# Optimization experiments

Hardware: AMD Instinct MI355X
Metric: run time of the kernel (lower is better)

The kernel has to match this reference:

```python
import jax, jax.numpy as jnp
import numpy as np

NUM_HEAD = 8   # in_channels // 64 for in_channels=512
DIM = 8        # per-head dim (== num_head in this module)
H_CH = NUM_HEAD * DIM  # 64
SCALE = DIM ** (-0.5)


def _conv(x, w, b, padding):
    # x: [N,C,H,W], w: [O,I,kh,kw]
    out = jax.lax.conv_general_dilated(
        x, w, window_strides=(1, 1), padding=padding,
        dimension_numbers=("NCHW", "OIHW", "NCHW"))
    return out + b[None, :, None, None]


def setup_inputs() -> dict:
    key = jax.random.key(0)
    ks = jax.random.split(key, 4)
    N, C, H, W = 4, 512, 48, 48
    x = jax.random.normal(ks[0], (N, C, H, W), dtype=jnp.float32)
    qkv_w = jax.random.normal(ks[1], (3 * H_CH, C, 1, 1), dtype=jnp.float32) * 0.05
    qkv_b = jnp.zeros((3 * H_CH,), dtype=jnp.float32)
    pos_w = jax.random.normal(ks[2], (H_CH, H_CH, 3, 3), dtype=jnp.float32) * 0.05
    pos_b = jnp.zeros((H_CH,), dtype=jnp.float32)
    res_w = jax.random.normal(ks[3], (C, H_CH, 1, 1), dtype=jnp.float32) * 0.05
    res_b = jnp.zeros((C,), dtype=jnp.float32)
    return {"x": x, "qkv_w": qkv_w, "qkv_b": qkv_b,
            "pos_w": pos_w, "pos_b": pos_b,
            "res_w": res_w, "res_b": res_b}


def reference(x, qkv_w, qkv_b, pos_w, pos_b, res_w, res_b):
    N, C, H, W = x.shape
    L = H * W
    # 1x1 conv QKV projection -> [N, 3h, H, W]
    qkv = _conv(x, qkv_w, qkv_b, "VALID")
    # [N, num_head, 3*dim, L]
    qkv = qkv.reshape(N, NUM_HEAD, 3 * DIM, L)
    q, k, v = qkv[:, :, :DIM], qkv[:, :, DIM:2 * DIM], qkv[:, :, 2 * DIM:]
    # attn = q^T @ k * scale : [N, nh, L, L], softmax over keys (last dim)
    attn = jnp.einsum("nhdq,nhdk->nhqk", q, k) * SCALE
    attn = jax.nn.softmax(attn, axis=-1)
    # out = v @ attn^T : [N, nh, dim, L]
    out = jnp.einsum("nhdk,nhqk->nhdq", v, attn)
    out = out.reshape(N, H_CH, H, W)
    # positional branch: 3x3 conv on v
    pos = _conv(v.reshape(N, H_CH, H, W), pos_w, pos_b, "SAME")
    out = out + pos
    # resume 1x1 conv -> [N, out_channels, H, W]
    return _conv(out, res_w, res_b, "VALID")
```

## Files before the change

### kernel.cpp

```cpp
#include <hip/hip_runtime.h>

#define L_ATT 2304
#define QSCALE_LOG2E 0.5100695712f

using bh8 = __attribute__((ext_vector_type(8))) short;
using f4  = __attribute__((ext_vector_type(4))) float;

#if __has_builtin(__builtin_amdgcn_exp2f)
#define EXP2(x) __builtin_amdgcn_exp2f(x)
#else
#define EXP2(x) exp2f(x)
#endif

__device__ inline short f2b(float f) {
    union { float f; unsigned u; } c; c.f = f;
    unsigned r = (c.u + 0x7FFFu + ((c.u >> 16) & 1u)) >> 16;
    return (short)r;
}
__device__ inline float b2f(short s) {
    union { unsigned u; float f; } c;
    c.u = ((unsigned)(unsigned short)s) << 16;
    return c.f;
}
__device__ inline int packhi(float lo, float hi) {
    return (int)__builtin_amdgcn_perm(__float_as_uint(hi), __float_as_uint(lo), 0x07060302u);
}
__device__ inline unsigned pk2(float lo, float hi) {
    return (unsigned)(unsigned short)f2b(lo) | ((unsigned)(unsigned short)f2b(hi) << 16);
}

__global__ __launch_bounds__(256) void prep_kernel(
    const float* __restrict__ qkv_w, const float* __restrict__ res_w,
    const float* __restrict__ pos_w, short* __restrict__ wqb,
    short* __restrict__ reswb, short* __restrict__ wqp)
{
    int j = blockIdx.x * 256 + threadIdx.x;
    if (j < 24576) {
        float4 v = ((const float4*)qkv_w)[j];
        short4 o = { f2b(v.x), f2b(v.y), f2b(v.z), f2b(v.w) };
        *(short4*)(wqb + (size_t)j * 4) = o;
    } else if (j < 32768) {
        int idx = j - 24576;
        float4 v = ((const float4*)res_w)[idx];
        short4 o = { f2b(v.x), f2b(v.y), f2b(v.z), f2b(v.w) };
        *(short4*)(reswb + (size_t)idx * 4) = o;
    } else {
        int e = j - 32768;
        wqp[e] = f2b(pos_w[(size_t)(e & 4095) * 9 + (e >> 12)]);
    }
}

__global__ __launch_bounds__(256) void qkv_kernel(
    const float* __restrict__ x, const short* __restrict__ wqb,
    const float* __restrict__ qkv_b, short* __restrict__ qt8,
    short* __restrict__ kt8, short* __restrict__ vt, short* __restrict__ vle)
{
    __shared__ short bs[32 * 520];
    const int g = blockIdx.x;
    const int xcd = g & 7, rr = g >> 3;
    const int y = rr % 3, grp = rr / 3;
    const int code = grp * 8 + xcd;
    const int l0 = (code % 72) * 32, oc0 = y * 64, n = code / 72;

    const int tid = threadIdx.x;
    const int lane = tid & 63, wave = tid >> 6;
    const int col = lane & 15, quad = lane >> 4;
    const int ocb = oc0 + wave * 16;

    {
        const float* src = x + (size_t)n * 512 * L_ATT + l0;
#pragma unroll
        for (int j = 0; j < 8; ++j) {
            int idx = j * 256 + tid;
            int k2 = (idx >> 3) * 2;
            int lq = (idx & 7) * 4;
            float4 av = *(const float4*)(src + (size_t)k2 * L_ATT + lq);
            float4 bv = *(const float4*)(src + (size_t)(k2 + 1) * L_ATT + lq);
            *(unsigned*)&bs[(lq + 0) * 520 + k2] = pk2(av.x, bv.x);
            *(unsigned*)&bs[(lq + 1) * 520 + k2] = pk2(av.y, bv.y);
            *(unsigned*)&bs[(lq + 2) * 520 + k2] = pk2(av.z, bv.z);
            *(unsigned*)&bs[(lq + 3) * 520 + k2] = pk2(av.w, bv.w);
        }
    }
    __syncthreads();

    f4 acc[2];
    acc[0] = (f4){0.f, 0.f, 0.f, 0.f};
    acc[1] = (f4){0.f, 0.f, 0.f, 0.f};

    const short* arow = wqb + (size_t)(ocb + col) * 512 + quad * 8;
    const short* b0p = bs + col * 520 + quad * 8;
    const short* b1p = b0p + 16 * 520;

#pragma unroll 4
    for (int k0 = 0; k0 < 512; k0 += 32) {
        bh8 af = *(const bh8*)(arow + k0);
        bh8 b0 = *(const bh8*)(b0p + k0);
        bh8 b1 = *(const bh8*)(b1p + k0);
        acc[0] = __builtin_amdgcn_mfma_f32_16x16x32_bf16(af, b0, acc[0], 0, 0, 0);
        acc[1] = __builtin_amdgcn_mfma_f32_16x16x32_bf16(af, b1, acc[1], 0, 0, 0);
    }

    const int obase = ocb + quad * 4;
    const int h = obase / 24;
    const int r0 = obase - h * 24;
    const int slice = n * 8 + h;

#pragma unroll
    for (int nt = 0; nt < 2; ++nt) {
        int l = l0 + nt * 16 + col;
        float v[4];
#pragma unroll
        for (int reg = 0; reg < 4; ++reg) v[reg] = acc[nt][reg] + qkv_b[obase + reg];
        if (r0 < 8) {
            short4 o = { f2b(v[0] * QSCALE_LOG2E), f2b(v[1] * QSCALE_LOG2E),
                         f2b(v[2] * QSCALE_LOG2E), f2b(v[3] * QSCALE_LOG2E) };
            *(short4*)(qt8 + ((size_t)slice * L_ATT + l) * 8 + r0) = o;
        } else if (r0 < 16) {
            short4 o = { f2b(v[0]), f2b(v[1]), f2b(v[2]), f2b(v[3]) };
            *(short4*)(kt8 + ((size_t)slice * L_ATT + l) * 8 + (r0 - 8)) = o;
        } else {
            short4 o = { f2b(v[0]), f2b(v[1]), f2b(v[2]), f2b(v[3]) };
            int d0 = r0 - 16;
#pragma unroll
            for (int reg = 0; reg < 4; ++reg)
                vt[((size_t)slice * 8 + d0 + reg) * L_ATT + l] = ((short*)&o)[reg];
            *(short4*)(vle + ((size_t)n * L_ATT + l) * 64 + h * 8 + d0) = o;
        }
    }
}

__global__ __launch_bounds__(256) void attnpos_kernel(
    const short* __restrict__ qt8, const short* __restrict__ kt8,
    const short* __restrict__ vt, const short* __restrict__ vle,
    const short* __restrict__ wqp, const float* __restrict__ pbias,
    float* __restrict__ pnum, float* __restrict__ pls, short* __restrict__ pcv)
{
    __shared__ short smem[6160];
    const int g = blockIdx.x;
    const int tid = threadIdx.x;
    const int lane = tid & 63, wave = tid >> 6;
    const int col = lane & 15, quad = lane >> 4;

    if (g < 1152) {
        const int h = g & 7, r = g >> 3;
        const int n = r / 36;
        const int rem = r - n * 36;
        const int qt = rem >> 1, half = rem & 1;
        const int q0 = qt * 128;
        const int kbase = half * 1152;
        const int slice = n * 8 + h;

        const short* qs  = qt8 + (size_t)slice * L_ATT * 8;
        const short* ks8 = kt8 + (size_t)slice * L_ATT * 8;
        const short* vb  = vt  + (size_t)slice * 8 * L_ATT;

        if (tid < 16) smem[6144 + tid] = (tid < 8) ? (short)0x3F80 : (short)0;

        bh8 zero8 = {0, 0, 0, 0, 0, 0, 0, 0};
        bh8 qf[2];
#pragma unroll
        for (int f = 0; f < 2; ++f) {
            qf[f] = zero8;
            if (quad == 0)
                qf[f] = *(const bh8*)(qs + (size_t)(q0 + wave * 32 + f * 16 + col) * 8);
        }

        int kidx[4];
#pragma unroll
        for (int nt = 0; nt < 4; ++nt)
            kidx[nt] = (quad == 0) ? (nt * 16 + col) * 8 : 6152;
        int vidx[2];
#pragma unroll
        for (int ks = 0; ks < 2; ++ks)
            vidx[ks] = (col < 8)
                     ? col * 64 + ((ks * 32 + quad * 8 + col * 8) & 63)
                     : ((col == 8) ? 6144 : 6152);

        const int ksl = ((lane >> 5) & 1) * 32 + ((lane >> 2) & 1) * 16
                      + ((lane >> 3) & 3) * 4 + (lane & 3);
        const int vd = lane >> 3, vkc = (lane & 7) * 8;
        const int vsl = vd * 64 + ((vkc + vd * 8) & 63);

        if (wave < 3)
            *(uint4*)&smem[wave * 512 + ksl * 8] =
                *(const uint4*)(ks8 + (size_t)(kbase + wave * 64 + lane) * 8);
        else
            *(uint4*)&smem[3072 + vsl] =
                *(const uint4*)(vb + (size_t)vd * L_ATT + kbase + vkc);
        if (wave == 0)
            *(uint4*)&smem[3072 + 512 + vsl] =
                *(const uint4*)(vb + (size_t)vd * L_ATT + kbase + 64 + vkc);
        else if (wave == 1)
            *(uint4*)&smem[3072 + 1024 + vsl] =
                *(const uint4*)(vb + (size_t)vd * L_ATT + kbase + 128 + vkc);
        __syncthreads();

        f4 oacc[2];
        oacc[0] = (f4){0.f, 0.f, 0.f, 0.f};
        oacc[1] = (f4){0.f, 0.f, 0.f, 0.f};

        int p = 0;
        for (int t = 0; t < 6; ++t) {
            uint4 dA, dB;
            if (wave < 3)
                dA = *(const uint4*)(ks8 + (size_t)(kbase + (t * 3 + 3 + wave) * 64 + lane) * 8);
            else
                dA = *(const uint4*)(vb + (size_t)vd * L_ATT + kbase + (t * 3 + 3) * 64 + vkc);
            if (wave == 0)
                dB = *(const uint4*)(vb + (size_t)vd * L_ATT + kbase + (t * 3 + 4) * 64 + vkc);
            else if (wave == 1)
                dB = *(const uint4*)(vb + (size_t)vd * L_ATT + kbase + (t * 3 + 5) * 64 + vkc);

#pragma unroll
            for (int u = 0; u < 3; ++u) {
                const int ku = (quad == 0) ? p * 1536 + u * 512 : 0;
                const int vu = (col < 8) ? 3072 + p * 1536 + u * 512 : 0;
                bh8 kf[4], vf[2];
#pragma unroll
                for (int nt = 0; nt < 4; ++nt) kf[nt] = *(const bh8*)&smem[kidx[nt] + ku];
#pragma unroll
                for (int ks = 0; ks < 2; ++ks) vf[ks] = *(const bh8*)&smem[vidx[ks] + vu];

                __builtin_amdgcn_s_setprio(1);
#pragma unroll
                for (int f = 0; f < 2; ++f) {
                    f4 s[4];
#pragma unroll
                    for (int nt = 0; nt < 4; ++nt) {
                        f4 z = (f4){0.f, 0.f, 0.f, 0.f};
                        s[nt] = __builtin_amdgcn_mfma_f32_16x16x32_bf16(kf[nt], qf[f], z, 0, 0, 0);
                    }
                    float e[4][4];
#pragma unroll
                    for (int nt = 0; nt < 4; ++nt)
#pragma unroll
                        for (int reg = 0; reg < 4; ++reg)
                            e[nt][reg] = EXP2(s[nt][reg]);
#pragma unroll
                    for (int ks = 0; ks < 2; ++ks) {
                        union { int i[4]; bh8 v; } pu;
                        pu.i[0] = packhi(e[2 * ks][0],     e[2 * ks][1]);
                        pu.i[1] = packhi(e[2 * ks][2],     e[2 * ks][3]);
                        pu.i[2] = packhi(e[2 * ks + 1][0], e[2 * ks + 1][1]);
                        pu.i[3] = packhi(e[2 * ks + 1][2], e[2 * ks + 1][3]);
                        oacc[f] = __builtin_amdgcn_mfma_f32_16x16x32_bf16(vf[ks], pu.v, oacc[f], 0, 0, 0);
                    }
                }
                __builtin_amdgcn_s_setprio(0);
            }

            if (wave < 3)
                *(uint4*)&smem[(p ^ 1) * 1536 + wave * 512 + ksl * 8] = dA;
            else
                *(uint4*)&smem[3072 + (p ^ 1) * 1536 + vsl] = dA;
            if (wave == 0)
                *(uint4*)&smem[3072 + (p ^ 1) * 1536 + 512 + vsl] = dB;
            else if (wave == 1)
                *(uint4*)&smem[3072 + (p ^ 1) * 1536 + 1024 + vsl] = dB;
            p ^= 1;
            __syncthreads();
        }

        const size_t prow = (size_t)(slice * 2 + half) * L_ATT;
#pragma unroll
        for (int f = 0; f < 2; ++f) {
            int qg = q0 + wave * 32 + f * 16 + col;
            if (quad < 2) {
                float4 o = { oacc[f][0], oacc[f][1], oacc[f][2], oacc[f][3] };
                *(float4*)(pnum + (prow + qg) * 8 + quad * 4) = o;
            } else if (quad == 2) {
                pls[prow + qg] = oacc[f][0];
            }
        }
        return;
    }

    const int gf = g - 1152;
    const int l0 = (gf % 144) * 16, n = gf / 144;
    const int t = wave;

    const int la = l0 + col;
    const int ya = la / 48, xa = la - ya * 48;

    f4 acc = (f4){0.f, 0.f, 0.f, 0.f};
    const short* vbase = vle + (size_t)n * L_ATT * 64;

#pragma unroll
    for (int q = 0; q < 9; ++q) {
        const int dy = q / 3 - 1, dx = q - (q / 3) * 3 - 1;
        const bool valid = ((unsigned)(ya + dy) < 48u) && ((unsigned)(xa + dx) < 48u);
        const short* ap = vbase + (size_t)(la + dy * 48 + dx) * 64 + quad * 8;
#pragma unroll
        for (int ks = 0; ks < 2; ++ks) {
            bh8 af = {0, 0, 0, 0, 0, 0, 0, 0};
            if (valid) af = *(const bh8*)(ap + ks * 32);
            bh8 bf = *(const bh8*)(wqp + ((size_t)q * 64 + t * 16 + col) * 64
                                   + ks * 32 + quad * 8);
            acc = __builtin_amdgcn_mfma_f32_16x16x32_bf16(af, bf, acc, 0, 0, 0);
        }
    }

    short* op = pcv + (size_t)n * L_ATT * 64;
    const int oc = t * 16 + col;
    const float bb = pbias[oc];
#pragma unroll
    for (int reg = 0; reg < 4; ++reg) {
        int l = l0 + quad * 4 + reg;
        op[(size_t)l * 64 + oc] = f2b(acc[reg] + bb);
    }
}

__global__ __launch_bounds__(256) void comb_kernel(
    const float* __restrict__ pnum, const float* __restrict__ pls,
    const short* __restrict__ pcv, short* __restrict__ battp)
{
    const int b = blockIdx.x;
    const int n = b / 144, lt = b % 144;
    const int hh = threadIdx.x & 15;
    const int l  = lt * 16 + (threadIdx.x >> 4);
    const int h = hh >> 1, dh = hh & 1;

    const size_t p0 = (size_t)((n * 8 + h) * 2) * L_ATT;
    const size_t p1 = p0 + L_ATT;
    float4 a = *(const float4*)(pnum + (p0 + l) * 8 + dh * 4);
    float4 c = *(const float4*)(pnum + (p1 + l) * 8 + dh * 4);
    float inv = 1.0f / (pls[p0 + l] + pls[p1 + l]);
    short4 pv = *(const short4*)(pcv + ((size_t)n * L_ATT + l) * 64 + hh * 4);

    int2 o;
    o.x = packhi((a.x + c.x) * inv + b2f(pv.x), (a.y + c.y) * inv + b2f(pv.y));
    o.y = packhi((a.z + c.z) * inv + b2f(pv.z), (a.w + c.w) * inv + b2f(pv.w));
    *(int2*)(battp + ((size_t)n * L_ATT + l) * 64 + hh * 4) = o;
}

__global__ __launch_bounds__(256) void res_kernel(
    const short* __restrict__ battp, const short* __restrict__ reswb,
    const float* __restrict__ res_b, float* __restrict__ out)
{
    const int g = blockIdx.x;
    const int xcd = g & 7, rr = g >> 3;
    const int y = rr & 7, grp = rr >> 3;
    const int code = grp * 8 + xcd;
    const int l0 = (code % 36) * 64, oc0 = y * 64, n = code / 36;

    const int lane = threadIdx.x & 63, wave = threadIdx.x >> 6;
    const int col = lane & 15, quad = lane >> 4;
    const int ocb = oc0 + wave * 16;

    f4 acc[4];
#pragma unroll
    for (int nt = 0; nt < 4; ++nt) acc[nt] = (f4){0.f, 0.f, 0.f, 0.f};

#pragma unroll
    for (int ks = 0; ks < 2; ++ks) {
        bh8 af = *(const bh8*)(reswb + (size_t)(ocb + col) * 64 + ks * 32 + quad * 8);
        const int ch = ks * 32 + quad * 8;
#pragma unroll
        for (int nt = 0; nt < 4; ++nt) {
            const int l = l0 + nt * 16 + col;
            bh8 bf = *(const bh8*)(battp + ((size_t)n * L_ATT + l) * 64 + ch);
            acc[nt] = __builtin_amdgcn_mfma_f32_16x16x32_bf16(af, bf, acc[nt], 0, 0, 0);
        }
    }

#pragma unroll
    for (int nt = 0; nt < 4; ++nt) {
        int l = l0 + nt * 16 + col;
#pragma unroll
        for (int reg = 0; reg < 4; ++reg) {
            int oc = ocb + quad * 4 + reg;
            out[((size_t)n * 512 + oc) * L_ATT + l] = acc[nt][reg] + res_b[oc];
        }
    }
}

extern "C" void kernel_launch(void* const* d_in, const int* in_sizes, int n_in,
                              void* d_out, int out_size, void* d_ws, size_t ws_size,
                              hipStream_t stream)
{
    const float* x      = (const float*)d_in[0];
    const float* qkv_w  = (const float*)d_in[1];
    const float* qkv_b  = (const float*)d_in[2];
    const float* pos_w  = (const float*)d_in[3];
    const float* pos_b  = (const float*)d_in[4];
    const float* res_w  = (const float*)d_in[5];
    const float* res_b  = (const float*)d_in[6];
    float* out = (float*)d_out;

    char* ws = (char*)d_ws;
    float* pnum  = (float*)(ws);
    float* pls   = (float*)(ws + 4718592);
    short* qt8   = (short*)(ws + 9437184);
    short* kt8   = (short*)(ws + 10616832);
    short* vt    = (short*)(ws + 11796480);
    short* pcv   = (short*)(ws + 12976128);
    short* wqb   = (short*)(ws + 14155776);
    short* reswb = (short*)(ws + 14352384);
    short* vle   = (short*)(ws + 14417920);
    short* wqp   = (short*)(ws + 15597568);
    short* battp = (short*)(ws + 15671296);

    prep_kernel<<<272, 256, 0, stream>>>(qkv_w, res_w, pos_w, wqb, reswb, wqp);
    qkv_kernel<<<864, 256, 0, stream>>>(x, wqb, qkv_b, qt8, kt8, vt, vle);
    attnpos_kernel<<<1728, 256, 0, stream>>>(qt8, kt8, vt, vle, wqp, pos_b, pnum, pls, pcv);
    comb_kernel<<<576, 256, 0, stream>>>(pnum, pls, pcv, battp);
    res_kernel<<<1152, 256, 0, stream>>>(battp, reswb, res_b, out);
}
```

Measured before the change: 132.4 us.

## Load whole K/V half-range into LDS once instead of double-buffered streaming

```diff
diff --git a/kernel.cpp b/kernel.cpp
--- a/kernel.cpp
+++ b/kernel.cpp
@@ -136,7 +136,7 @@
     const short* __restrict__ wqp, const float* __restrict__ pbias,
     float* __restrict__ pnum, float* __restrict__ pls, short* __restrict__ pcv)
 {
-    __shared__ short smem[6160];
+    __shared__ short smem[18448];
     const int g = blockIdx.x;
     const int tid = threadIdx.x;
     const int lane = tid & 63, wave = tid >> 6;
@@ -155,7 +155,7 @@
         const short* ks8 = kt8 + (size_t)slice * L_ATT * 8;
         const short* vb  = vt  + (size_t)slice * 8 * L_ATT;
 
-        if (tid < 16) smem[6144 + tid] = (tid < 8) ? (short)0x3F80 : (short)0;
+        if (tid < 16) smem[18432 + tid] = (tid < 8) ? (short)0x3F80 : (short)0;
 
         bh8 zero8 = {0, 0, 0, 0, 0, 0, 0, 0};
         bh8 qf[2];
@@ -169,97 +169,66 @@
         int kidx[4];
 #pragma unroll
         for (int nt = 0; nt < 4; ++nt)
-            kidx[nt] = (quad == 0) ? (nt * 16 + col) * 8 : 6152;
+            kidx[nt] = (quad == 0) ? (nt * 16 + col) * 8 : 18440;
         int vidx[2];
 #pragma unroll
         for (int ks = 0; ks < 2; ++ks)
             vidx[ks] = (col < 8)
-                     ? col * 64 + ((ks * 32 + quad * 8 + col * 8) & 63)
-                     : ((col == 8) ? 6144 : 6152);
+                     ? 9216 + col * 64 + ((ks * 32 + quad * 8 + col * 8) & 63)
+                     : ((col == 8) ? 18432 : 18440);
 
         const int ksl = ((lane >> 5) & 1) * 32 + ((lane >> 2) & 1) * 16
                       + ((lane >> 3) & 3) * 4 + (lane & 3);
         const int vd = lane >> 3, vkc = (lane & 7) * 8;
         const int vsl = vd * 64 + ((vkc + vd * 8) & 63);
 
-        if (wave < 3)
-            *(uint4*)&smem[wave * 512 + ksl * 8] =
-                *(const uint4*)(ks8 + (size_t)(kbase + wave * 64 + lane) * 8);
-        else
-            *(uint4*)&smem[3072 + vsl] =
-                *(const uint4*)(vb + (size_t)vd * L_ATT + kbase + vkc);
-        if (wave == 0)
-            *(uint4*)&smem[3072 + 512 + vsl] =
-                *(const uint4*)(vb + (size_t)vd * L_ATT + kbase + 64 + vkc);
-        else if (wave == 1)
-            *(uint4*)&smem[3072 + 1024 + vsl] =
-                *(const uint4*)(vb + (size_t)vd * L_ATT + kbase + 128 + vkc);
+        for (int s = wave; s < 18; s += 4)
+            *(uint4*)&smem[s * 512 + ksl * 8] =
+                *(const uint4*)(ks8 + (size_t)(kbase + s * 64 + lane) * 8);
+        for (int s = wave; s < 18; s += 4)
+            *(uint4*)&smem[9216 + s * 512 + vsl] =
+                *(const uint4*)(vb + (size_t)vd * L_ATT + kbase + s * 64 + vkc);
         __syncthreads();
 
         f4 oacc[2];
         oacc[0] = (f4){0.f, 0.f, 0.f, 0.f};
         oacc[1] = (f4){0.f, 0.f, 0.f, 0.f};
 
-        int p = 0;
-        for (int t = 0; t < 6; ++t) {
-            uint4 dA, dB;
-            if (wave < 3)
-                dA = *(const uint4*)(ks8 + (size_t)(kbase + (t * 3 + 3 + wave) * 64 + lane) * 8);
-            else
-                dA = *(const uint4*)(vb + (size_t)vd * L_ATT + kbase + (t * 3 + 3) * 64 + vkc);
-            if (wave == 0)
-                dB = *(const uint4*)(vb + (size_t)vd * L_ATT + kbase + (t * 3 + 4) * 64 + vkc);
-            else if (wave == 1)
-                dB = *(const uint4*)(vb + (size_t)vd * L_ATT + kbase + (t * 3 + 5) * 64 + vkc);
-
-#pragma unroll
-            for (int u = 0; u < 3; ++u) {
-                const int ku = (quad == 0) ? p * 1536 + u * 512 : 0;
-                const int vu = (col < 8) ? 3072 + p * 1536 + u * 512 : 0;
-                bh8 kf[4], vf[2];
-#pragma unroll
-                for (int nt = 0; nt < 4; ++nt) kf[nt] = *(const bh8*)&smem[kidx[nt] + ku];
-#pragma unroll
-                for (int ks = 0; ks < 2; ++ks) vf[ks] = *(const bh8*)&smem[vidx[ks] + vu];
-
-                __builtin_amdgcn_s_setprio(1);
-#pragma unroll
-                for (int f = 0; f < 2; ++f) {
-                    f4 s[4];
-#pragma unroll
-                    for (int nt = 0; nt < 4; ++nt) {
-                        f4 z = (f4){0.f, 0.f, 0.f, 0.f};
-                        s[nt] = __builtin_amdgcn_mfma_f32_16x16x32_bf16(kf[nt], qf[f], z, 0, 0, 0);
-                    }
-                    float e[4][4];
-#pragma unroll
-                    for (int nt = 0; nt < 4; ++nt)
-#pragma unroll
-                        for (int reg = 0; reg < 4; ++reg)
-                            e[nt][reg] = EXP2(s[nt][reg]);
-#pragma unroll
-                    for (int ks = 0; ks < 2; ++ks) {
-                        union { int i[4]; bh8 v; } pu;
-                        pu.i[0] = packhi(e[2 * ks][0],     e[2 * ks][1]);
-                        pu.i[1] = packhi(e[2 * ks][2],     e[2 * ks][3]);
-                        pu.i[2] = packhi(e[2 * ks + 1][0], e[2 * ks + 1][1]);
-                        pu.i[3] = packhi(e[2 * ks + 1][2], e[2 * ks + 1][3]);
-                        oacc[f] = __builtin_amdgcn_mfma_f32_16x16x32_bf16(vf[ks], pu.v, oacc[f], 0, 0, 0);
-                    }
+        for (int s = 0; s < 18; ++s) {
+            const int ku = (quad == 0) ? s * 512 : 0;
+            const int vu = (col < 8) ? s * 512 : 0;
+            bh8 kf[4], vf[2];
+#pragma unroll
+            for (int nt = 0; nt < 4; ++nt) kf[nt] = *(const bh8*)&smem[kidx[nt] + ku];
+#pragma unroll
+            for (int ks = 0; ks < 2; ++ks) vf[ks] = *(const bh8*)&smem[vidx[ks] + vu];
+
+            __builtin_amdgcn_s_setprio(1);
+#pragma unroll
+            for (int f = 0; f < 2; ++f) {
+                f4 sS[4];
+#pragma unroll
+                for (int nt = 0; nt < 4; ++nt) {
+                    f4 z = (f4){0.f, 0.f, 0.f, 0.f};
+                    sS[nt] = __builtin_amdgcn_mfma_f32_16x16x32_bf16(kf[nt], qf[f], z, 0, 0, 0);
                 }
-                __builtin_amdgcn_s_setprio(0);
+                float e[4][4];
+#pragma unroll
+                for (int nt = 0; nt < 4; ++nt)
+#pragma unroll
+                    for (int reg = 0; reg < 4; ++reg)
+                        e[nt][reg] = EXP2(sS[nt][reg]);
+#pragma unroll
+                for (int ks = 0; ks < 2; ++ks) {
+                    union { int i[4]; bh8 v; } pu;
+                    pu.i[0] = packhi(e[2 * ks][0],     e[2 * ks][1]);
+                    pu.i[1] = packhi(e[2 * ks][2],     e[2 * ks][3]);
+                    pu.i[2] = packhi(e[2 * ks + 1][0], e[2 * ks + 1][1]);
+                    pu.i[3] = packhi(e[2 * ks + 1][2], e[2 * ks + 1][3]);
+                    oacc[f] = __builtin_amdgcn_mfma_f32_16x16x32_bf16(vf[ks], pu.v, oacc[f], 0, 0, 0);
+                }
             }
-
-            if (wave < 3)
-                *(uint4*)&smem[(p ^ 1) * 1536 + wave * 512 + ksl * 8] = dA;
-            else
-                *(uint4*)&smem[3072 + (p ^ 1) * 1536 + vsl] = dA;
-            if (wave == 0)
-                *(uint4*)&smem[3072 + (p ^ 1) * 1536 + 512 + vsl] = dB;
-            else if (wave == 1)
-                *(uint4*)&smem[3072 + (p ^ 1) * 1536 + 1024 + vsl] = dB;
-            p ^= 1;
-            __syncthreads();
+            __builtin_amdgcn_s_setprio(0);
         }
 
         const size_t prow = (size_t)(slice * 2 + half) * L_ATT;
```

Result: no change. 133.9 us (+1.2%).
